# Optimization experiments

Measured on AMD Instinct MI355X. Metric: run time of the kernel, lower is better.

Reference implementation:

```python
import jax, jax.numpy as jnp
import numpy as np

IOU_THRESHOLDS = (0.5, 0.75)
B, N, G = 256, 4000, 50


def _iou(amin, amax, bmin, bmax):
    # broadcasted temporal IoU: anchors [N,1] vs boxes [1,G] -> [N,G]
    inter = jnp.maximum(jnp.minimum(amax, bmax) - jnp.maximum(amin, bmin), 0.0)
    union = (amax - amin) + (bmax - bmin) - inter
    return inter / union


def _greedy_tp(segments, gts, thr):
    # segments: [N,2], gts: [G,2]. Replicates AP.get_values greedy matching:
    # for each label (in order), claim the first (lowest-index) unused proposal
    # whose IoU > thr. Final used-mask == is_TP.
    ious = _iou(segments[:, 0:1], segments[:, 1:2], gts[None, :, 0], gts[None, :, 1])  # [N,G]
    pot = ious > thr
    n = segments.shape[0]

    def step(used, col):  # col: [N] bool, candidates for this label
        cand = col & ~used
        idx = jnp.argmax(cand)  # first True (argmax of bool is first max)
        used = jnp.where(jnp.any(cand), used.at[idx].set(True), used)
        return used, None

    used, _ = jax.lax.scan(step, jnp.zeros((n,), jnp.bool_), pot.T)
    return used  # [N] bool


def _ap_for_threshold(scores, segments, labels, thr):
    is_tp = jax.vmap(lambda s, g: _greedy_tp(s, g, thr))(segments, labels)  # [B,N]
    conf = scores.reshape(-1)                       # [B*N]
    tp = is_tp.reshape(-1).astype(jnp.float32)
    order = jnp.argsort(-conf)                      # sort by confidence, descending
    tp = tp[order]
    n_labels = labels.shape[0] * labels.shape[1]
    m = tp.shape[0]
    acc_tp = jnp.cumsum(tp)
    precision = acc_tp / (jnp.arange(m, dtype=jnp.float32) + 1.0)
    recall = acc_tp / jnp.float32(n_labels)
    # curve = [[1,0]] then (recall, precision) reversed; AP = sum(|dx| * cummax(y)[:-1])
    x = jnp.concatenate([jnp.ones((1,), jnp.float32), recall[::-1]])
    y = jnp.concatenate([jnp.zeros((1,), jnp.float32), precision[::-1]])
    y_max = jax.lax.cummax(y, axis=0)
    x_diff = jnp.abs(jnp.diff(x))
    return jnp.sum(x_diff * y_max[:-1])


def setup_inputs() -> dict:
    key = jax.random.key(0)
    k1, k2, k3, k4, k5 = jax.random.split(key, 5)
    scores = jax.random.uniform(k1, (B, N), dtype=jnp.float32)
    p_start = jax.random.uniform(k2, (B, N), dtype=jnp.float32) * 0.9
    p_len = jax.random.uniform(k3, (B, N), dtype=jnp.float32) * 0.1 + 0.005
    segments = jnp.stack([p_start, p_start + p_len], axis=-1)  # [B,N,2], start<end
    g_start = jax.random.uniform(k4, (B, G), dtype=jnp.float32) * 0.9
    g_len = jax.random.uniform(k5, (B, G), dtype=jnp.float32) * 0.1 + 0.005
    labels = jnp.stack([g_start, g_start + g_len], axis=-1)    # [B,G,2]
    return {"scores": scores, "segments": segments, "labels": labels}


def reference(scores, segments, labels):
    # returns AP at each IoU threshold, shape [len(IOU_THRESHOLDS)]
    return jnp.stack([_ap_for_threshold(scores, segments, labels, t) for t in IOU_THRESHOLDS])
```

## Files before the change

kernel.cpp:

```cpp
#include <hip/hip_runtime.h>


#define B_ 256
#define N_ 4000
#define G_ 50
#define M_ (B_ * N_)
#define NL_ (B_ * G_)
#define NBKT 2048

#define M0_ 0x1.000001p-1
#define M1_ 0x1.800001p-1

typedef unsigned long long u64;

__device__ __forceinline__ unsigned bucket_of(float c) {
    unsigned b = (unsigned)(c * 2048.0f);
    return b > (NBKT - 1) ? (NBKT - 1) : b;
}

__global__ __launch_bounds__(1024) void tp_kernel(
    const float* __restrict__ seg,
    const float* __restrict__ gts,
    const float* __restrict__ conf,
    int* __restrict__ tpIdx,
    int* __restrict__ cnt,
    unsigned short* __restrict__ pbh)
{
    const int tid  = threadIdx.x;
    const int lane = tid & 63;
    const int wv   = tid >> 6;
    const int b    = blockIdx.x;

    __shared__ float2 gtl[G_];
    __shared__ u64 cand[2][G_][64];
    __shared__ unsigned hls[NBKT];
    __shared__ int lcnt[2];

    #pragma unroll
    for (int k = 0; k < NBKT / 1024; ++k) hls[k * 1024 + tid] = 0u;
    if (tid < G_) gtl[tid] = ((const float2*)gts)[b * G_ + tid];
    if (tid < 2) lcnt[tid] = 0;
    __syncthreads();

    const float* cb = conf + (size_t)b * N_;
    #pragma unroll
    for (int s = 0; s < 4; ++s) {
        int n = s * 1024 + tid;
        if (n < N_) atomicAdd(&hls[bucket_of(cb[n])], 1u);
    }

    const float2* sb = (const float2*)(seg + (size_t)b * (N_ * 2));
    float pmin[4], pmax[4], plen[4];
    #pragma unroll
    for (int s = 0; s < 4; ++s) {
        int n = s * 1024 + tid;
        if (n < N_) { float2 v = sb[n]; pmin[s] = v.x; pmax[s] = v.y; }
        else { pmin[s] = 1e9f; pmax[s] = 1e9f; }
        plen[s] = pmax[s] - pmin[s];
    }
    for (int g = 0; g < G_; ++g) {
        float2 gt = gtl[g];
        float glen = gt.y - gt.x;
        u64 m0[4], m1[4];
        #pragma unroll
        for (int s = 0; s < 4; ++s) {
            float inter = fmaxf(fminf(pmax[s], gt.y) - fmaxf(pmin[s], gt.x), 0.0f);
            float uni = plen[s] + glen - inter;
            double di = (double)inter;
            double du = (double)uni;
            m0[s] = __ballot(di > M0_ * du);
            m1[s] = __ballot(di > M1_ * du);
        }
        if (lane == 0) {
            #pragma unroll
            for (int s = 0; s < 4; ++s) {
                cand[0][g][s * 16 + wv] = m0[s];
                cand[1][g][s * 16 + wv] = m1[s];
            }
        }
    }
    __syncthreads();

    #pragma unroll
    for (int k = 0; k < NBKT / 1024; ++k) {
        int bin = k * 1024 + tid;
        pbh[(size_t)b * NBKT + bin] = (unsigned short)hls[bin];
    }

    if (wv < 2) {
        const int thr_i = wv;
        u64 used = 0ull;
        for (int g = 0; g < G_; ++g) {
            u64 c = cand[thr_i][g][lane] & ~used;
            u64 ball = __ballot(c != 0ull);
            if (ball) {
                int fl = __ffsll(ball) - 1;
                if (lane == fl) used |= (c & (0ull - c));
            }
        }
        int cpop = __popcll(used);
        if (cpop) {
            int j = atomicAdd(&lcnt[thr_i], cpop);
            u64 u = used;
            while (u) {
                int bit = __ffsll(u) - 1;
                u &= u - 1;
                tpIdx[thr_i * NL_ + b * G_ + j++] = b * N_ + lane * 64 + bit;
            }
        }
    }
    __syncthreads();
    if (tid < 2) cnt[tid * B_ + b] = lcnt[tid];
}

__global__ __launch_bounds__(256) void s1_kernel(
    unsigned short* __restrict__ pbh,
    unsigned* __restrict__ total)
{
    __shared__ unsigned short tile[256][32];
    const int j = blockIdx.x;
    const int t = threadIdx.x;
    uint4* dst = (uint4*)&tile[t][0];
    const uint4* src = (const uint4*)(pbh + (size_t)t * NBKT + j * 32);
    #pragma unroll
    for (int k = 0; k < 4; ++k) dst[k] = src[k];
    __syncthreads();
    if (t < 32) {
        unsigned run = 0;
        for (int b = 0; b < 256; ++b) {
            unsigned v = tile[b][t];
            tile[b][t] = (unsigned short)run;
            run += v;
        }
        total[j * 32 + t] = run;
    }
    __syncthreads();
    uint4* back = (uint4*)(pbh + (size_t)t * NBKT + j * 32);
    #pragma unroll
    for (int k = 0; k < 4; ++k) back[k] = dst[k];
}

__global__ __launch_bounds__(1024) void scatter_kernel(
    const float* __restrict__ conf,
    const unsigned short* __restrict__ pbh,
    const unsigned* __restrict__ total,
    unsigned* __restrict__ binStartG,
    u64* __restrict__ sKey)
{
    __shared__ unsigned baseB[NBKT];
    __shared__ unsigned lofs[NBKT];
    const int tid = threadIdx.x;
    const int b = blockIdx.x;

    unsigned* part = lofs;
    uint2 v2 = ((const uint2*)total)[tid];
    unsigned s = v2.x + v2.y;
    part[tid] = s;
    __syncthreads();
    for (int off = 1; off < 1024; off <<= 1) {
        unsigned add = (tid >= off) ? part[tid - off] : 0u;
        __syncthreads();
        part[tid] += add;
        __syncthreads();
    }
    unsigned base = (tid == 0) ? 0u : part[tid - 1];
    __syncthreads();
    baseB[2 * tid]     = base;
    baseB[2 * tid + 1] = base + v2.x;
    __syncthreads();
    #pragma unroll
    for (int k = 0; k < 2; ++k) {
        int bin = k * 1024 + tid;
        unsigned bs = baseB[bin];
        if (b == 0) binStartG[bin] = bs;
        baseB[bin] = bs + pbh[(size_t)b * NBKT + bin];
        lofs[bin] = 0u;
    }
    __syncthreads();

    const float* cb = conf + (size_t)b * N_;
    #pragma unroll
    for (int s4 = 0; s4 < 4; ++s4) {
        int n = s4 * 1024 + tid;
        if (n < N_) {
            float c = cb[n];
            unsigned bin = bucket_of(c);
            unsigned lo = atomicAdd(&lofs[bin], 1u);
            unsigned idx = (unsigned)(b * N_ + n);
            sKey[baseB[bin] + lo] = ((u64)__float_as_uint(c) << 32) | (u64)(0xFFFFFFFFu - idx);
        }
    }
}

__global__ __launch_bounds__(256) void rank_kernel(
    const float* __restrict__ conf,
    const int* __restrict__ tpIdx,
    const int* __restrict__ cnt,
    const unsigned* __restrict__ total,
    const unsigned* __restrict__ binStart,
    const u64* __restrict__ sKey,
    int* __restrict__ tpRank)
{
    const int lane = threadIdx.x & 63;
    const int w = (blockIdx.x << 2) | (threadIdx.x >> 6);
    if (w >= 2 * NL_) return;
    const int thr_i = w / NL_;
    const int t = w - thr_i * NL_;
    const int batch = t / G_;
    const int j = t - batch * G_;

    if (j < cnt[thr_i * B_ + batch]) {
        int e = tpIdx[thr_i * NL_ + t];
        float c = conf[e];
        u64 keyE = ((u64)__float_as_uint(c) << 32) | (u64)(0xFFFFFFFFu - (unsigned)e);
        unsigned bin = bucket_of(c);
        unsigned lo = binStart[bin], n = total[bin];
        int r = M_ - (int)lo - (int)n;
        for (unsigned base = 0; base < n; base += 64) {
            unsigned k = base + lane;
            bool pred = (k < n) && (sKey[lo + k] > keyE);
            r += (int)__popcll(__ballot(pred));
        }
        if (lane == 0) tpRank[thr_i * NL_ + t] = r;
    } else {
        if (lane == 0) tpRank[thr_i * NL_ + t] = M_ + t;
    }
}

__global__ __launch_bounds__(1024) void sortap_kernel(
    const int* __restrict__ tpRank,
    float* __restrict__ out)
{
    const int C = 13;
    union U1 { unsigned part[1024]; float cmax[1024]; };
    union U2 { unsigned hist[NBKT]; double red[1024]; };
    __shared__ int sr[NL_];
    __shared__ U1 u1;
    __shared__ U2 u2;
    const int thr_i = blockIdx.x;
    const int t = threadIdx.x;

    u2.hist[t] = 0u; u2.hist[t + 1024] = 0u;
    __syncthreads();

    int r[C]; unsigned beta[C];
    #pragma unroll
    for (int k = 0; k < C; ++k) {
        int i = t + k * 1024;
        if (i < NL_) {
            int rr = tpRank[thr_i * NL_ + i];
            r[k] = rr;
            unsigned bb = ((unsigned)rr) >> 9;
            beta[k] = bb > (NBKT - 1) ? (NBKT - 1) : bb;
            atomicAdd(&u2.hist[beta[k]], 1u);
        } else { r[k] = 0; beta[k] = 0xFFFFFFFFu; }
    }
    __syncthreads();

    unsigned h0 = u2.hist[2 * t], h1 = u2.hist[2 * t + 1];
    u1.part[t] = h0 + h1;
    __syncthreads();
    for (int off = 1; off < 1024; off <<= 1) {
        unsigned add = (t >= off) ? u1.part[t - off] : 0u;
        __syncthreads();
        u1.part[t] += add;
        __syncthreads();
    }
    unsigned base = (t == 0) ? 0u : u1.part[t - 1];
    __syncthreads();
    u2.hist[2 * t] = base;
    u2.hist[2 * t + 1] = base + h0;
    __syncthreads();

    #pragma unroll
    for (int k = 0; k < C; ++k)
        if (beta[k] != 0xFFFFFFFFu) {
            unsigned slot = atomicAdd(&u2.hist[beta[k]], 1u);
            sr[slot] = r[k];
        }
    __syncthreads();

    int p[C];
    #pragma unroll
    for (int k = 0; k < C; ++k) {
        if (beta[k] != 0xFFFFFFFFu) {
            unsigned st = (beta[k] == 0u) ? 0u : u2.hist[beta[k] - 1];
            unsigned en = u2.hist[beta[k]];
            int c = 0;
            for (unsigned j = st; j < en; ++j) c += (sr[j] < r[k]);
            p[k] = (int)st + c;
        } else p[k] = -1;
    }
    __syncthreads();
    #pragma unroll
    for (int k = 0; k < C; ++k)
        if (p[k] >= 0) sr[p[k]] = r[k];
    __syncthreads();

    float pr[C]; int rk[C];
    #pragma unroll
    for (int k = 0; k < C; ++k) {
        int i = t * C + k;
        rk[k] = (i < NL_) ? sr[i] : 0x7FFFFFFF;
        pr[k] = (rk[k] < M_) ? (float)(i + 1) / (float)(rk[k] + 1) : -1.0f;
    }
    float suf[C];
    float run = -1.0f;
    #pragma unroll
    for (int k = C - 1; k >= 0; --k) { run = fmaxf(run, pr[k]); suf[k] = run; }

    u1.cmax[t] = run;
    __syncthreads();
    for (int off = 1; off < 1024; off <<= 1) {
        float v = u1.cmax[t];
        float o = (t + off < 1024) ? u1.cmax[t + off] : -1.0f;
        __syncthreads();
        u1.cmax[t] = fmaxf(v, o);
        __syncthreads();
    }
    float follow = (t + 1 < 1024) ? u1.cmax[t + 1] : -1.0f;

    double acc = 0.0;
    #pragma unroll
    for (int k = 0; k < C; ++k) {
        int i = t * C + k;
        if (rk[k] >= 1 && rk[k] < M_) {
            float smax = fmaxf(suf[k], follow);
            float rhi = (float)(i + 1) / 12800.0f;
            float rlo = (float)i / 12800.0f;
            acc += (double)((rhi - rlo) * smax);
        }
    }
    __syncthreads();
    u2.red[t] = acc;
    __syncthreads();
    for (int off = 512; off >= 1; off >>= 1) {
        if (t < off) u2.red[t] += u2.red[t + off];
        __syncthreads();
    }
    if (t == 0) out[thr_i] = (float)u2.red[0];
}

extern "C" void kernel_launch(void* const* d_in, const int* in_sizes, int n_in,
                              void* d_out, int out_size, void* d_ws, size_t ws_size,
                              hipStream_t stream) {
    const float* scores = (const float*)d_in[0];
    const float* seg    = (const float*)d_in[1];
    const float* gts    = (const float*)d_in[2];
    float* out = (float*)d_out;

    char* p = (char*)d_ws;
    int*            cnt        = (int*)p;             p += 4096;
    int*            tpIdx      = (int*)p;             p += 2 * NL_ * 4;
    int*            tpRank     = (int*)p;             p += 2 * NL_ * 4;
    unsigned*       total      = (unsigned*)p;        p += NBKT * 4;
    unsigned*       binStart   = (unsigned*)p;        p += NBKT * 4;
    unsigned short* pbh        = (unsigned short*)p;  p += (size_t)B_ * NBKT * 2;
    u64*            sKey       = (u64*)p;             p += (size_t)M_ * 8;
    (void)ws_size; (void)in_sizes; (void)n_in; (void)out_size;

    tp_kernel<<<B_, 1024, 0, stream>>>(seg, gts, scores, tpIdx, cnt, pbh);
    s1_kernel<<<64, 256, 0, stream>>>(pbh, total);
    scatter_kernel<<<B_, 1024, 0, stream>>>(scores, pbh, total, binStart, sKey);
    rank_kernel<<<(2 * NL_ + 3) / 4, 256, 0, stream>>>(scores, tpIdx, cnt,
                                                       total, binStart, sKey, tpRank);
    sortap_kernel<<<2, 1024, 0, stream>>>(tpRank, out);
}
```

Measured before the change: 168.1 us.

## Double confidence buckets, pack 16-bit histogram counts, replace fp64 IoU tests with fp32

The confidence histogram grows from 2048 to 4096 buckets. Counts are packed as two 16-bit halves per shared-memory word so the shared footprint stays the same, and the scan and scatter kernels are widened to match. Finer buckets are meant to shrink per-bucket work in the rank kernel. The double-precision IoU threshold comparisons become single-precision difference tests with a small epsilon, removing slow fp64 math in tp_kernel, at some risk of exactness at the threshold boundary.

```diff
diff --git a/kernel.cpp b/kernel.cpp
--- a/kernel.cpp
+++ b/kernel.cpp
@@ -6,15 +6,13 @@
 #define G_ 50
 #define M_ (B_ * N_)
 #define NL_ (B_ * G_)
-#define NBKT 2048
-
-#define M0_ 0x1.000001p-1
-#define M1_ 0x1.800001p-1
+#define NBKT 4096
+#define SBKT 2048
 
 typedef unsigned long long u64;
 
 __device__ __forceinline__ unsigned bucket_of(float c) {
-    unsigned b = (unsigned)(c * 2048.0f);
+    unsigned b = (unsigned)(c * 4096.0f);
     return b > (NBKT - 1) ? (NBKT - 1) : b;
 }
 
@@ -33,11 +31,11 @@
 
     __shared__ float2 gtl[G_];
     __shared__ u64 cand[2][G_][64];
-    __shared__ unsigned hls[NBKT];
+    __shared__ unsigned hls[NBKT / 2];
     __shared__ int lcnt[2];
 
     #pragma unroll
-    for (int k = 0; k < NBKT / 1024; ++k) hls[k * 1024 + tid] = 0u;
+    for (int k = 0; k < NBKT / 2048; ++k) hls[k * 1024 + tid] = 0u;
     if (tid < G_) gtl[tid] = ((const float2*)gts)[b * G_ + tid];
     if (tid < 2) lcnt[tid] = 0;
     __syncthreads();
@@ -46,7 +44,10 @@
     #pragma unroll
     for (int s = 0; s < 4; ++s) {
         int n = s * 1024 + tid;
-        if (n < N_) atomicAdd(&hls[bucket_of(cb[n])], 1u);
+        if (n < N_) {
+            unsigned bin = bucket_of(cb[n]);
+            atomicAdd(&hls[bin >> 1], 1u << ((bin & 1) * 16));
+        }
     }
 
     const float2* sb = (const float2*)(seg + (size_t)b * (N_ * 2));
@@ -66,10 +67,10 @@
         for (int s = 0; s < 4; ++s) {
             float inter = fmaxf(fminf(pmax[s], gt.y) - fmaxf(pmin[s], gt.x), 0.0f);
             float uni = plen[s] + glen - inter;
-            double di = (double)inter;
-            double du = (double)uni;
-            m0[s] = __ballot(di > M0_ * du);
-            m1[s] = __ballot(di > M1_ * du);
+            float e25 = uni * 0x1p-25f;
+            float d   = inter - 0.5f * uni;
+            m0[s] = __ballot(d > e25);
+            m1[s] = __ballot((d - 0.25f * uni) > e25);
         }
         if (lane == 0) {
             #pragma unroll
@@ -81,10 +82,11 @@
     }
     __syncthreads();
 
-    #pragma unroll
-    for (int k = 0; k < NBKT / 1024; ++k) {
-        int bin = k * 1024 + tid;
-        pbh[(size_t)b * NBKT + bin] = (unsigned short)hls[bin];
+    {
+        unsigned* prow = (unsigned*)(pbh + (size_t)b * NBKT);
+        #pragma unroll
+        for (int k = 0; k < NBKT / 2048; ++k)
+            prow[k * 1024 + tid] = hls[k * 1024 + tid];
     }
 
     if (wv < 2) {
@@ -153,8 +155,8 @@
     const int b = blockIdx.x;
 
     unsigned* part = lofs;
-    uint2 v2 = ((const uint2*)total)[tid];
-    unsigned s = v2.x + v2.y;
+    uint4 v4 = ((const uint4*)total)[tid];
+    unsigned s = v4.x + v4.y + v4.z + v4.w;
     part[tid] = s;
     __syncthreads();
     for (int off = 1; off < 1024; off <<= 1) {
@@ -165,11 +167,13 @@
     }
     unsigned base = (tid == 0) ? 0u : part[tid - 1];
     __syncthreads();
-    baseB[2 * tid]     = base;
-    baseB[2 * tid + 1] = base + v2.x;
-    __syncthreads();
-    #pragma unroll
-    for (int k = 0; k < 2; ++k) {
+    baseB[4 * tid]     = base;
+    baseB[4 * tid + 1] = base + v4.x;
+    baseB[4 * tid + 2] = base + v4.x + v4.y;
+    baseB[4 * tid + 3] = base + v4.x + v4.y + v4.z;
+    __syncthreads();
+    #pragma unroll
+    for (int k = 0; k < 4; ++k) {
         int bin = k * 1024 + tid;
         unsigned bs = baseB[bin];
         if (b == 0) binStartG[bin] = bs;
@@ -233,7 +237,7 @@
 {
     const int C = 13;
     union U1 { unsigned part[1024]; float cmax[1024]; };
-    union U2 { unsigned hist[NBKT]; double red[1024]; };
+    union U2 { unsigned hist[SBKT]; double red[1024]; };
     __shared__ int sr[NL_];
     __shared__ U1 u1;
     __shared__ U2 u2;
@@ -251,7 +255,7 @@
             int rr = tpRank[thr_i * NL_ + i];
             r[k] = rr;
             unsigned bb = ((unsigned)rr) >> 9;
-            beta[k] = bb > (NBKT - 1) ? (NBKT - 1) : bb;
+            beta[k] = bb > (SBKT - 1) ? (SBKT - 1) : bb;
             atomicAdd(&u2.hist[beta[k]], 1u);
         } else { r[k] = 0; beta[k] = 0xFFFFFFFFu; }
     }
@@ -360,7 +364,7 @@
     (void)ws_size; (void)in_sizes; (void)n_in; (void)out_size;
 
     tp_kernel<<<B_, 1024, 0, stream>>>(seg, gts, scores, tpIdx, cnt, pbh);
-    s1_kernel<<<64, 256, 0, stream>>>(pbh, total);
+    s1_kernel<<<NBKT / 32, 256, 0, stream>>>(pbh, total);
     scatter_kernel<<<B_, 1024, 0, stream>>>(scores, pbh, total, binStart, sKey);
     rank_kernel<<<(2 * NL_ + 3) / 4, 256, 0, stream>>>(scores, tpIdx, cnt,
                                                        total, binStart, sKey, tpRank);
```

New measurement: 163.8 us. -2.6%, faster.
